# Performance work log

Hardware: AMD Instinct MI355X
Metric: run time of the kernel (lower is better)

## Reference

```python
import jax, jax.numpy as jnp
import numpy as np

MARGIN = 1.0
ALPHA = 0.5
EPS = 1e-12  # sqrt-smoothing epsilon (keeps grads finite on the zero diagonal)


def _pairwise_d2(x):
    # x: [B, D] -> squared euclidean distance matrix [B, B]
    sq = jnp.sum(x * x, axis=-1)
    return jnp.maximum(sq[:, None] + sq[None, :] - 2.0 * (x @ x.T), 0.0)


def setup_inputs() -> dict:
    key = jax.random.key(0)
    k1, k2 = jax.random.split(key)
    N, B, D = 32, 1024, 1024
    outputs = jax.random.normal(k1, (N, B, D), dtype=jnp.float32)
    encode_sentences = jax.random.normal(k2, (B, D), dtype=jnp.float32)
    return {"outputs": outputs, "encode_sentences": encode_sentences}


def reference(outputs, encode_sentences):
    # outputs: [N, B, D] (N secrets, batch B, embed D); encode_sentences: [B, D]
    N, B, D = outputs.shape

    # --- sentence (distance-consistency) loss ---
    # original: mean_i MSE( pdist(outputs[i]), pdist(encode_sentences) )
    d_sent = jnp.sqrt(_pairwise_d2(encode_sentences) + EPS)          # [B, B]
    d_out = jnp.sqrt(jax.vmap(_pairwise_d2)(outputs) + EPS)          # [N, B, B]
    # mean over N of per-i means == global mean (all terms same size B*B)
    sentence_loss = jnp.mean((d_out - d_sent[None]) ** 2)

    # --- secret (pairwise margin) loss ---
    # original: sum_{i<j} mean_b relu(margin - ||outputs[i,b] - outputs[j,b]||)
    x = jnp.swapaxes(outputs, 0, 1)                                   # [B, N, D]
    sq = jnp.sum(x * x, axis=-1)                                      # [B, N]
    gram = jnp.einsum('bnd,bmd->bnm', x, x)                           # [B, N, N]
    d2 = jnp.maximum(sq[:, :, None] + sq[:, None, :] - 2.0 * gram, 0.0)
    d = jnp.sqrt(d2 + EPS)                                            # [B, N, N]
    hinge = jax.nn.relu(MARGIN - d)                                   # [B, N, N]
    upper = jnp.triu(jnp.ones((N, N), dtype=bool), k=1)               # i < j mask
    secret_distance = jnp.sum(jnp.where(upper[None], hinge, 0.0)) / B
    n_pairs = N * (N - 1) / 2.0
    secret_loss = secret_distance / n_pairs

    loss = ALPHA * sentence_loss + (1.0 - ALPHA) * secret_loss
    return (loss, sentence_loss, secret_loss)
```

## Files before the change

### kernel.cpp

```cpp
#include <hip/hip_runtime.h>
#include <hip/hip_bf16.h>

#define N_SEC 32
#define BDIM 1024
#define DDIM 1024

typedef __attribute__((ext_vector_type(8))) short bf16x8;
typedef __attribute__((ext_vector_type(4))) float f32x4;
typedef __attribute__((ext_vector_type(4))) int i32x4;

#define WAITVM(n) asm volatile("s_waitcnt vmcnt(" #n ")" ::: "memory")

__device__ __forceinline__ void bar() {
    __builtin_amdgcn_s_barrier();
    asm volatile("" ::: "memory");
}

__device__ __forceinline__ unsigned pk2(float a, float b) {
    union { __hip_bfloat162 h; unsigned u; } cv;
    cv.h = __float22bfloat162_rn(make_float2(a, b));
    return cv.u;
}

__device__ __forceinline__ i32x4 pack8(float4 a, float4 b) {
    i32x4 r;
    r[0] = pk2(a.x, a.y); r[1] = pk2(a.z, a.w);
    r[2] = pk2(b.x, b.y); r[3] = pk2(b.z, b.w);
    return r;
}

__device__ __forceinline__ f32x4 mfma16(bf16x8 a, bf16x8 b, f32x4 c) {
    return __builtin_amdgcn_mfma_f32_16x16x32_bf16(a, b, c, 0, 0, 0);
}

__device__ __forceinline__ float wave_sum(float v) {
    #pragma unroll
    for (int off = 32; off > 0; off >>= 1) v += __shfl_down(v, off, 64);
    return v;
}

__device__ __forceinline__ void gload16(const unsigned short* g, unsigned short* l) {
    __builtin_amdgcn_global_load_lds(
        (const __attribute__((address_space(1))) unsigned int*)g,
        (__attribute__((address_space(3))) unsigned int*)l, 16, 0, 0);
}


__global__ void prep_k(const float* __restrict__ outp, const float* __restrict__ enc,
                       unsigned short* __restrict__ Xb, unsigned short* __restrict__ Eb,
                       float* __restrict__ sq_out, float* __restrict__ sq_enc) {
    int wid = threadIdx.x >> 6, l = threadIdx.x & 63;
    int r = blockIdx.x * 4 + wid;
    bool isOut = r < N_SEC * BDIM;
    const float* src = isOut ? (outp + (size_t)r * DDIM)
                             : (enc + (size_t)(r - N_SEC * BDIM) * DDIM);
    unsigned short* dst = isOut ? (Xb + (size_t)r * DDIM)
                                : (Eb + (size_t)(r - N_SEC * BDIM) * DDIM);
    const float4* s4 = (const float4*)src;
    float s = 0.f;
    #pragma unroll
    for (int h = 0; h < 2; ++h) {
        int c = l + h * 64;
        float4 v0 = s4[2 * c], v1 = s4[2 * c + 1];
        i32x4 p = pack8(v0, v1);
        *(i32x4*)&dst[c * 8] = p;
        #pragma unroll
        for (int e = 0; e < 4; ++e) {
            unsigned u = (unsigned)p[e];
            float a = __uint_as_float(u << 16);
            float b = __uint_as_float(u & 0xFFFF0000u);
            s += a * a + b * b;
        }
    }
    s = wave_sum(s);
    if (l == 0) { if (isOut) sq_out[r] = s; else sq_enc[r - N_SEC * BDIM] = s; }
}

__global__ void zero_k(float* __restrict__ p) {
    int i = blockIdx.x * blockDim.x + threadIdx.x;
    float4 z = {0.f, 0.f, 0.f, 0.f};
    ((float4*)p)[i] = z;
    ((float4*)p)[i + 131072] = z;
}

__global__ void cvt0_k(float* __restrict__ d, const float* __restrict__ sq) {
    int t = blockIdx.x * blockDim.x + threadIdx.x;
    #pragma unroll
    for (int h = 0; h < 2; ++h) {
        int idx = t + h * 131072;
        int i = idx >> 8;
        float si = sq[i];
        float4 g = ((const float4*)d)[idx];
        int j0 = (idx & 255) * 4;
        float4 r;
        r.x = sqrtf(fmaxf(si + sq[j0 + 0] - 2.f * g.x, 0.f) + 1e-12f);
        r.y = sqrtf(fmaxf(si + sq[j0 + 1] - 2.f * g.y, 0.f) + 1e-12f);
        r.z = sqrtf(fmaxf(si + sq[j0 + 2] - 2.f * g.z, 0.f) + 1e-12f);
        r.w = sqrtf(fmaxf(si + sq[j0 + 3] - 2.f * g.w, 0.f) + 1e-12f);
        ((float4*)d)[idx] = r;
    }
}

template<int MODE, int NIT>
__global__ void gram8_k(const unsigned short* __restrict__ Xb, const float* __restrict__ sqv,
                        const float* __restrict__ dsent_r, float* __restrict__ dsent_w,
                        float* __restrict__ partials, int kbeg_base) {
    int n, tile, kbeg;
    if (MODE == 1) {
        int g = blockIdx.x;
        int xcd = g & 7, local = g >> 3;
        n = xcd * 4 + local / 36;
        tile = local % 36;
        kbeg = 0;
    } else {
        n = 0;
        tile = blockIdx.x >> 2;
        kbeg = (blockIdx.x & 3) * NIT;
        (void)kbeg_base;
    }
    int idx = tile, ti = 0;
    while (idx >= 8 - ti) { idx -= 8 - ti; ti++; }
    int tj = ti + idx;
    const unsigned short* Xn = Xb + (size_t)n * BDIM * DDIM;
    const float* sqn = sqv + n * BDIM;
    int i0 = ti * 128, j0 = tj * 128;
    bool diag = (ti == tj);

    __shared__ __align__(16) unsigned short Ash[3][4096];
    __shared__ __align__(16) unsigned short Bsh[3][4096];
    __shared__ float red[4];

    int t = threadIdx.x, wid = t >> 6, l = t & 63;
    int wr = wid >> 1, wc = wid & 1;
    bool dead = diag && (wr > wc);
    int cg = l >> 4, lr = l & 15;

    f32x4 acc[4][4];
    #pragma unroll
    for (int a = 0; a < 4; a++)
        #pragma unroll
        for (int c = 0; c < 4; c++) acc[a][c] = f32x4{0.f, 0.f, 0.f, 0.f};

    int eoffA[4], eoffB[4];
    #pragma unroll
    for (int f = 0; f < 4; f++) {
        int ra = wr * 64 + f * 16 + lr;
        eoffA[f] = ra * 32 + ((cg ^ ((ra >> 1) & 3)) * 8);
        int rb = wc * 64 + f * 16 + lr;
        eoffB[f] = rb * 32 + ((cg ^ ((rb >> 1) & 3)) * 8);
    }

    int rs = wid * 16 + (l >> 2);
    int cgs = (l & 3) ^ ((rs >> 1) & 3);
    const unsigned short* gA0 = Xn + (size_t)(i0 + rs) * DDIM + cgs * 8;
    const unsigned short* gA1 = gA0 + (size_t)64 * DDIM;
    const unsigned short* gB0 = Xn + (size_t)(j0 + rs) * DDIM + cgs * 8;
    const unsigned short* gB1 = gB0 + (size_t)64 * DDIM;

    auto stage = [&](int buf, int kt) {
        int ko = kt * 32;
        gload16(gA0 + ko, &Ash[buf][wid * 512]);
        gload16(gA1 + ko, &Ash[buf][2048 + wid * 512]);
        gload16(gB0 + ko, &Bsh[buf][wid * 512]);
        gload16(gB1 + ko, &Bsh[buf][2048 + wid * 512]);
    };
    auto compute = [&](int buf) {
        if (dead) return;
        bf16x8 af[4], bfr[4];
        #pragma unroll
        for (int f = 0; f < 4; f++) {
            af[f]  = *(const bf16x8*)&Ash[buf][eoffA[f]];
            bfr[f] = *(const bf16x8*)&Bsh[buf][eoffB[f]];
        }
        #pragma unroll
        for (int fi = 0; fi < 4; fi++)
            #pragma unroll
            for (int fj = 0; fj < 4; fj++) {
                if (diag && wr == wc && fj < fi) continue;
                acc[fi][fj] = mfma16(af[fi], bfr[fj], acc[fi][fj]);
            }
    };

    int klast = kbeg + NIT - 1;
#define GSTEP(SB, CB) do {                       \
        int nx = c + 1; if (nx > klast) nx = klast; \
        stage(SB, nx);                           \
        WAITVM(4);                               \
        bar();                                   \
        compute(CB);                             \
        ++c; } while (0)

    stage(0, kbeg);
    int c = kbeg;
    #pragma unroll 1
    for (int it = 0; it < NIT / 3; ++it) {
        GSTEP(1, 0);
        GSTEP(2, 1);
        GSTEP(0, 2);
    }
    if (NIT % 3 >= 1) GSTEP(1, 0);
    if (NIT % 3 >= 2) GSTEP(2, 1);
#undef GSTEP
    asm volatile("s_waitcnt vmcnt(0)" ::: "memory");

    float lsum = 0.f;
    if (!dead) {
        #pragma unroll
        for (int fi = 0; fi < 4; fi++) {
            #pragma unroll
            for (int fj = 0; fj < 4; fj++) {
                if (diag && wr == wc && fj < fi) continue;
                int jg = j0 + wc * 64 + fj * 16 + lr;
                #pragma unroll
                for (int e = 0; e < 4; e++) {
                    int ig = i0 + wr * 64 + fi * 16 + cg * 4 + e;
                    float g = acc[fi][fj][e];
                    if (MODE == 2) {
                        atomicAdd(&dsent_w[(size_t)ig * BDIM + jg], g);
                    } else {
                        float d2 = sqn[ig] + sqn[jg] - 2.f * g;
                        float d = sqrtf(fmaxf(d2, 0.f) + 1e-12f);
                        if (!diag || jg > ig) {
                            float diff = d - dsent_r[(size_t)ig * BDIM + jg];
                            lsum += diff * diff;
                        }
                    }
                }
            }
        }
    }
    if (MODE == 1) {
        lsum = wave_sum(lsum * 2.f);
        if (l == 0) red[wid] = lsum;
        __syncthreads();
        if (t == 0) partials[blockIdx.x] = red[0] + red[1] + red[2] + red[3];
    }
}

__global__ void secret4_k(const unsigned short* __restrict__ Xb,
                          const float* __restrict__ sq_out, float* __restrict__ partials) {
    __shared__ __align__(16) unsigned short S[2][32 * 4 * 128];
    __shared__ float red[4];
    int t = threadIdx.x, wid = t >> 6, l = t & 63;
    int b0 = blockIdx.x * 4;
    int cg = l >> 4, lr = l & 15;
    f32x4 a00 = {0.f,0.f,0.f,0.f}, a01 = {0.f,0.f,0.f,0.f}, a11 = {0.f,0.f,0.f,0.f};

    auto stage = [&](int buf, int kt) {
        #pragma unroll
        for (int m = 0; m < 8; ++m) {
            int n = m * 4 + wid;
            gload16(Xb + ((size_t)(n * BDIM + b0 + cg)) * DDIM + kt * 128 + ((lr ^ (n & 7)) * 8),
                    &S[buf][n * 512]);
        }
    };
    auto compute = [&](int buf) {
        #pragma unroll
        for (int k2 = 0; k2 < 4; ++k2) {
            int cs = k2 * 4 + cg;
            int cl = (cs ^ (lr & 7)) * 8;
            bf16x8 u0 = *(const bf16x8*)&S[buf][lr * 512 + wid * 128 + cl];
            bf16x8 u1 = *(const bf16x8*)&S[buf][(16 + lr) * 512 + wid * 128 + cl];
            a00 = mfma16(u0, u0, a00);
            a01 = mfma16(u0, u1, a01);
            a11 = mfma16(u1, u1, a11);
        }
    };

    stage(0, 0);
    __syncthreads();
    for (int kt = 0; kt < 6; kt += 2) {
        stage(1, kt + 1);
        compute(0);
        __syncthreads();
        stage(0, kt + 2);
        compute(1);
        __syncthreads();
    }
    stage(1, 7);
    compute(0);
    __syncthreads();
    compute(1);

    float lsum = 0.f;
    int b = b0 + wid;
    auto proc = [&](const f32x4& acc, int rb, int cb) {
        #pragma unroll
        for (int e = 0; e < 4; e++) {
            int i = rb * 16 + cg * 4 + e;
            int j = cb * 16 + lr;
            if (j > i) {
                float d2 = sq_out[(size_t)i * BDIM + b] + sq_out[(size_t)j * BDIM + b] - 2.f * acc[e];
                float d = sqrtf(fmaxf(d2, 0.f) + 1e-12f);
                lsum += fmaxf(1.f - d, 0.f);
            }
        }
    };
    proc(a00, 0, 0); proc(a01, 0, 1); proc(a11, 1, 1);
    lsum = wave_sum(lsum);
    if (l == 0) red[wid] = lsum;
    __syncthreads();
    if (t == 0) partials[blockIdx.x] = red[0] + red[1] + red[2] + red[3];
}

__global__ void fin2_k(const float* __restrict__ ps, const float* __restrict__ psec,
                       float* __restrict__ out) {
    __shared__ float red[16];
    int t = threadIdx.x;
    float s = 0.f;
    for (int i = t; i < 36 * N_SEC; i += 256) s += ps[i];
    float s2 = psec[t];
    s = wave_sum(s);
    s2 = wave_sum(s2);
    if ((t & 63) == 0) { red[t >> 6] = s; red[8 + (t >> 6)] = s2; }
    __syncthreads();
    if (t == 0) {
        float a = red[0] + red[1] + red[2] + red[3];
        float b = red[8] + red[9] + red[10] + red[11];
        float sl = a * (1.0f / 33554432.0f);
        float sec = b * (1.0f / (1024.0f * 496.0f));
        out[0] = 0.5f * sl + 0.5f * sec;
        out[1] = sl;
        out[2] = sec;
    }
}


__global__ void norms_k(const float* __restrict__ outp, const float* __restrict__ enc,
                        float* __restrict__ sq_out, float* __restrict__ sq_enc) {
    int wid = threadIdx.x >> 6, l = threadIdx.x & 63;
    int r = blockIdx.x * 4 + wid;
    const float* src = (r < N_SEC * BDIM) ? (outp + (size_t)r * DDIM)
                                          : (enc + (size_t)(r - N_SEC * BDIM) * DDIM);
    float s = 0.f;
    #pragma unroll
    for (int q = 0; q < 4; q++) {
        float4 v = reinterpret_cast<const float4*>(src)[l + q * 64];
        unsigned u0 = pk2(v.x, v.y), u1 = pk2(v.z, v.w);
        float a = __uint_as_float(u0 << 16), b = __uint_as_float(u0 & 0xFFFF0000u);
        float c = __uint_as_float(u1 << 16), d = __uint_as_float(u1 & 0xFFFF0000u);
        s += a * a + b * b + c * c + d * d;
    }
    s = wave_sum(s);
    if (l == 0) { if (r < N_SEC * BDIM) sq_out[r] = s; else sq_enc[r - N_SEC * BDIM] = s; }
}

template<int MODE>
__global__ void gram_k(const float* __restrict__ X, const float* __restrict__ sqv,
                       const float* __restrict__ dsent_r, float* __restrict__ dsent_w,
                       float* __restrict__ accum) {
    int idx = blockIdx.x, ti = 0;
    while (idx >= 8 - ti) { idx -= 8 - ti; ti++; }
    int tj = ti + idx;
    int n = (MODE == 1) ? blockIdx.y : 0;
    const float* Xn = X + (size_t)n * BDIM * DDIM;
    const float* sqn = sqv + n * BDIM;
    int i0 = ti * 128, j0 = tj * 128;
    bool diag = (ti == tj);
    __shared__ __align__(16) unsigned short Ash[128 * 32];
    __shared__ __align__(16) unsigned short Bsh[128 * 32];
    int t = threadIdx.x, wid = t >> 6, l = t & 63;
    int wr = wid >> 1, wc = wid & 1;
    bool dead = diag && (wr > wc);
    int cg = l >> 4, lr = l & 15;
    f32x4 acc[4][4];
    #pragma unroll
    for (int a = 0; a < 4; a++)
        #pragma unroll
        for (int c = 0; c < 4; c++) acc[a][c] = f32x4{0.f, 0.f, 0.f, 0.f};
    int r0 = t >> 2, c0 = t & 3;
    int swz0 = (c0 ^ (r0 & 3)) * 8;
    int off0 = r0 * 32 + swz0;
    int off1 = (r0 + 64) * 32 + swz0;
    for (int kt = 0; kt < DDIM / 32; ++kt) {
        int k0 = kt * 32;
        const float4* pa0 = (const float4*)(Xn + (size_t)(i0 + r0) * DDIM + k0 + c0 * 8);
        const float4* pa1 = (const float4*)(Xn + (size_t)(i0 + r0 + 64) * DDIM + k0 + c0 * 8);
        const float4* pb0 = (const float4*)(Xn + (size_t)(j0 + r0) * DDIM + k0 + c0 * 8);
        const float4* pb1 = (const float4*)(Xn + (size_t)(j0 + r0 + 64) * DDIM + k0 + c0 * 8);
        float4 a00 = pa0[0], a01 = pa0[1];
        float4 a10 = pa1[0], a11 = pa1[1];
        float4 b00 = pb0[0], b01 = pb0[1];
        float4 b10 = pb1[0], b11 = pb1[1];
        __syncthreads();
        *(i32x4*)&Ash[off0] = pack8(a00, a01);
        *(i32x4*)&Ash[off1] = pack8(a10, a11);
        *(i32x4*)&Bsh[off0] = pack8(b00, b01);
        *(i32x4*)&Bsh[off1] = pack8(b10, b11);
        __syncthreads();
        if (!dead) {
            bf16x8 af[4], bfr[4];
            #pragma unroll
            for (int f = 0; f < 4; f++) {
                int ra = wr * 64 + f * 16 + lr;
                af[f] = *(const bf16x8*)&Ash[ra * 32 + ((cg ^ (ra & 3)) * 8)];
                int rb = wc * 64 + f * 16 + lr;
                bfr[f] = *(const bf16x8*)&Bsh[rb * 32 + ((cg ^ (rb & 3)) * 8)];
            }
            #pragma unroll
            for (int fi = 0; fi < 4; fi++)
                #pragma unroll
                for (int fj = 0; fj < 4; fj++) {
                    if (diag && wr == wc && fj < fi) continue;
                    acc[fi][fj] = mfma16(af[fi], bfr[fj], acc[fi][fj]);
                }
        }
    }
    if (!dead) {
        float lsum = 0.f;
        #pragma unroll
        for (int fi = 0; fi < 4; fi++) {
            #pragma unroll
            for (int fj = 0; fj < 4; fj++) {
                if (diag && wr == wc && fj < fi) continue;
                int jg = j0 + wc * 64 + fj * 16 + lr;
                #pragma unroll
                for (int e = 0; e < 4; e++) {
                    int ig = i0 + wr * 64 + fi * 16 + cg * 4 + e;
                    float g = acc[fi][fj][e];
                    float d2 = sqn[ig] + sqn[jg] - 2.f * g;
                    float d = sqrtf(fmaxf(d2, 0.f) + 1e-12f);
                    if (MODE == 0) {
                        dsent_w[(size_t)ig * BDIM + jg] = d;
                    } else {
                        if (!diag || jg > ig) {
                            float diff = d - dsent_r[(size_t)ig * BDIM + jg];
                            lsum += diff * diff;
                        }
                    }
                }
            }
        }
        if (MODE == 1) {
            lsum = wave_sum(lsum * 2.f);
            if (l == 0) atomicAdd(accum, lsum);
        }
    }
}

__global__ void secret_k(const float* __restrict__ X, const float* __restrict__ sq_out,
                         float* __restrict__ accum) {
    int wid = threadIdx.x >> 6, l = threadIdx.x & 63;
    int b = blockIdx.x * 4 + wid;
    int cg = l >> 4, lr = l & 15;
    f32x4 a00 = {0.f,0.f,0.f,0.f}, a01 = {0.f,0.f,0.f,0.f}, a11 = {0.f,0.f,0.f,0.f};
    for (int kt = 0; kt < 32; ++kt) {
        int k0 = kt * 32 + cg * 8;
        const float4* p0 = (const float4*)(X + ((size_t)lr * BDIM + b) * DDIM + k0);
        const float4* p1 = (const float4*)(X + ((size_t)(16 + lr) * BDIM + b) * DDIM + k0);
        union { i32x4 i; bf16x8 s; } u0, u1;
        u0.i = pack8(p0[0], p0[1]);
        u1.i = pack8(p1[0], p1[1]);
        a00 = mfma16(u0.s, u0.s, a00);
        a01 = mfma16(u0.s, u1.s, a01);
        a11 = mfma16(u1.s, u1.s, a11);
    }
    float lsum = 0.f;
    auto proc = [&](const f32x4& acc, int rb, int cb) {
        #pragma unroll
        for (int e = 0; e < 4; e++) {
            int i = rb * 16 + cg * 4 + e;
            int j = cb * 16 + lr;
            if (j > i) {
                float d2 = sq_out[(size_t)i * BDIM + b] + sq_out[(size_t)j * BDIM + b] - 2.f * acc[e];
                float d = sqrtf(fmaxf(d2, 0.f) + 1e-12f);
                lsum += fmaxf(1.f - d, 0.f);
            }
        }
    };
    proc(a00, 0, 0); proc(a01, 0, 1); proc(a11, 1, 1);
    lsum = wave_sum(lsum);
    if (l == 0) atomicAdd(accum, lsum);
}

__global__ void init_k(float* sums) { sums[threadIdx.x] = 0.f; }

__global__ void fin_k(const float* __restrict__ sums, float* __restrict__ out) {
    float sl = sums[0] * (1.0f / 33554432.0f);
    float sec = sums[1] * (1.0f / (1024.0f * 496.0f));
    out[0] = 0.5f * sl + 0.5f * sec;
    out[1] = sl;
    out[2] = sec;
}

extern "C" void kernel_launch(void* const* d_in, const int* in_sizes, int n_in,
                              void* d_out, int out_size, void* d_ws, size_t ws_size,
                              hipStream_t stream) {
    const float* outputs = (const float*)d_in[0];
    const float* enc     = (const float*)d_in[1];
    float* out = (float*)d_out;

    float* ps     = (float*)d_ws;
    float* psec   = ps + 1536;
    float* sq_out = ps + 2048;
    float* sq_enc = sq_out + N_SEC * BDIM;
    float* dsent  = sq_enc + BDIM;
    unsigned short* Xbf = (unsigned short*)(dsent + (size_t)BDIM * BDIM);
    unsigned short* Ebf = Xbf + (size_t)N_SEC * BDIM * DDIM;

    const size_t NEED = 4 * (2048 + (size_t)N_SEC * BDIM + BDIM + (size_t)BDIM * BDIM)
                      + 2 * ((size_t)N_SEC * BDIM * DDIM + (size_t)BDIM * DDIM);

    if (ws_size >= NEED) {
        hipLaunchKernelGGL(prep_k, dim3((N_SEC * BDIM + BDIM) / 4), dim3(256), 0, stream,
                           outputs, enc, Xbf, Ebf, sq_out, sq_enc);
        hipLaunchKernelGGL(zero_k, dim3(512), dim3(256), 0, stream, dsent);
        hipLaunchKernelGGL((gram8_k<2, 8>), dim3(36 * 4), dim3(256), 0, stream,
                           Ebf, sq_enc, (const float*)nullptr, dsent, (float*)nullptr, 0);
        hipLaunchKernelGGL(cvt0_k, dim3(512), dim3(256), 0, stream, dsent, sq_enc);
        hipLaunchKernelGGL((gram8_k<1, 32>), dim3(36 * N_SEC), dim3(256), 0, stream,
                           Xbf, sq_out, (const float*)dsent, (float*)nullptr, ps, 0);
        hipLaunchKernelGGL(secret4_k, dim3(BDIM / 4), dim3(256), 0, stream,
                           Xbf, sq_out, psec);
        hipLaunchKernelGGL(fin2_k, dim3(1), dim3(256), 0, stream, ps, psec, out);
    } else {
        float* sums = (float*)d_ws;
        float* fsq_out = sums + 64;
        float* fsq_enc = fsq_out + N_SEC * BDIM;
        float* fdsent  = fsq_enc + BDIM;
        hipLaunchKernelGGL(init_k, dim3(1), dim3(2), 0, stream, sums);
        hipLaunchKernelGGL(norms_k, dim3((N_SEC * BDIM + BDIM) / 4), dim3(256), 0, stream,
                           outputs, enc, fsq_out, fsq_enc);
        hipLaunchKernelGGL((gram_k<0>), dim3(36), dim3(256), 0, stream,
                           enc, fsq_enc, (const float*)nullptr, fdsent, (float*)nullptr);
        hipLaunchKernelGGL((gram_k<1>), dim3(36, N_SEC), dim3(256), 0, stream,
                           outputs, fsq_out, (const float*)fdsent, (float*)nullptr, &sums[0]);
        hipLaunchKernelGGL(secret_k, dim3(BDIM / 4), dim3(256), 0, stream,
                           outputs, fsq_out, &sums[1]);
        hipLaunchKernelGGL(fin_k, dim3(1), dim3(1), 0, stream, sums, out);
    }
}
```

Before: 146.9 us.

## Replace triangular 128-tile gram kernel with full 256x256 tiles, 8 waves, 64-wide K

The per-secret gram and distance-loss kernel changes from 36 triangular 128x128 tiles per secret, which skipped mirrored work, to 16 full 256x256 tiles with 512 threads. Each block now uses a double-buffered, interleaved staging schedule with a 64-wide K step, XOR-swizzled LDS and raised wave priority around the MFMAs. The goal is more data reuse per loaded byte and fewer blocks, at the cost of roughly 1.8x the MFMA work, since the symmetric half is no longer skipped. To support this, the sentence gram kernel now writes a full symmetric distance matrix and the final reduction reads a fixed 512 partials.

```diff
diff --git a/kernel.cpp b/kernel.cpp
--- a/kernel.cpp
+++ b/kernel.cpp
@@ -43,6 +43,37 @@
     __builtin_amdgcn_global_load_lds(
         (const __attribute__((address_space(1))) unsigned int*)g,
         (__attribute__((address_space(3))) unsigned int*)l, 16, 0, 0);
+}
+
+__device__ __forceinline__ void rdA(bf16x8 af[2][2], const unsigned short* base,
+                                    int FI0, int lr, int s0, int s1) {
+    #pragma unroll
+    for (int a2 = 0; a2 < 2; ++a2) {
+        int ro = ((FI0 + a2) * 16 + lr) * 64;
+        af[a2][0] = *(const bf16x8*)(base + ro + s0);
+        af[a2][1] = *(const bf16x8*)(base + ro + s1);
+    }
+}
+__device__ __forceinline__ void rdB(bf16x8 bq[4][2], const unsigned short* base,
+                                    int rbase, int lr, int s0, int s1) {
+    #pragma unroll
+    for (int fj = 0; fj < 4; ++fj) {
+        int ro = (rbase + fj * 16 + lr) * 64;
+        bq[fj][0] = *(const bf16x8*)(base + ro + s0);
+        bq[fj][1] = *(const bf16x8*)(base + ro + s1);
+    }
+}
+__device__ __forceinline__ void mm16(f32x4 acc[8][4], const bf16x8 af[2][2],
+                                     const bf16x8 bq[4][2], int FI0) {
+    __builtin_amdgcn_s_setprio(1);
+    #pragma unroll
+    for (int kk = 0; kk < 2; ++kk)
+        #pragma unroll
+        for (int a2 = 0; a2 < 2; ++a2)
+            #pragma unroll
+            for (int fj = 0; fj < 4; ++fj)
+                acc[FI0 + a2][fj] = mfma16(af[a2][kk], bq[fj][kk], acc[FI0 + a2][fj]);
+    __builtin_amdgcn_s_setprio(0);
 }
 
 
@@ -101,34 +132,19 @@
     }
 }
 
-template<int MODE, int NIT>
-__global__ void gram8_k(const unsigned short* __restrict__ Xb, const float* __restrict__ sqv,
-                        const float* __restrict__ dsent_r, float* __restrict__ dsent_w,
-                        float* __restrict__ partials, int kbeg_base) {
-    int n, tile, kbeg;
-    if (MODE == 1) {
-        int g = blockIdx.x;
-        int xcd = g & 7, local = g >> 3;
-        n = xcd * 4 + local / 36;
-        tile = local % 36;
-        kbeg = 0;
-    } else {
-        n = 0;
-        tile = blockIdx.x >> 2;
-        kbeg = (blockIdx.x & 3) * NIT;
-        (void)kbeg_base;
-    }
+template<int NIT>
+__global__ void gramE_k(const unsigned short* __restrict__ Xb, float* __restrict__ gw) {
+    int tile = blockIdx.x >> 2;
+    int kbeg = (blockIdx.x & 3) * NIT;
     int idx = tile, ti = 0;
     while (idx >= 8 - ti) { idx -= 8 - ti; ti++; }
     int tj = ti + idx;
-    const unsigned short* Xn = Xb + (size_t)n * BDIM * DDIM;
-    const float* sqn = sqv + n * BDIM;
+    const unsigned short* Xn = Xb;
     int i0 = ti * 128, j0 = tj * 128;
     bool diag = (ti == tj);
 
     __shared__ __align__(16) unsigned short Ash[3][4096];
     __shared__ __align__(16) unsigned short Bsh[3][4096];
-    __shared__ float red[4];
 
     int t = threadIdx.x, wid = t >> 6, l = t & 63;
     int wr = wid >> 1, wc = wid & 1;
@@ -149,7 +165,6 @@
         int rb = wc * 64 + f * 16 + lr;
         eoffB[f] = rb * 32 + ((cg ^ ((rb >> 1) & 3)) * 8);
     }
-
     int rs = wid * 16 + (l >> 2);
     int cgs = (l & 3) ^ ((rs >> 1) & 3);
     const unsigned short* gA0 = Xn + (size_t)(i0 + rs) * DDIM + cgs * 8;
@@ -189,24 +204,18 @@
         bar();                                   \
         compute(CB);                             \
         ++c; } while (0)
-
     stage(0, kbeg);
     int c = kbeg;
     #pragma unroll 1
-    for (int it = 0; it < NIT / 3; ++it) {
-        GSTEP(1, 0);
-        GSTEP(2, 1);
-        GSTEP(0, 2);
-    }
+    for (int it = 0; it < NIT / 3; ++it) { GSTEP(1, 0); GSTEP(2, 1); GSTEP(0, 2); }
     if (NIT % 3 >= 1) GSTEP(1, 0);
     if (NIT % 3 >= 2) GSTEP(2, 1);
 #undef GSTEP
     asm volatile("s_waitcnt vmcnt(0)" ::: "memory");
 
-    float lsum = 0.f;
     if (!dead) {
         #pragma unroll
-        for (int fi = 0; fi < 4; fi++) {
+        for (int fi = 0; fi < 4; fi++)
             #pragma unroll
             for (int fj = 0; fj < 4; fj++) {
                 if (diag && wr == wc && fj < fi) continue;
@@ -215,25 +224,128 @@
                 for (int e = 0; e < 4; e++) {
                     int ig = i0 + wr * 64 + fi * 16 + cg * 4 + e;
                     float g = acc[fi][fj][e];
-                    if (MODE == 2) {
-                        atomicAdd(&dsent_w[(size_t)ig * BDIM + jg], g);
-                    } else {
-                        float d2 = sqn[ig] + sqn[jg] - 2.f * g;
-                        float d = sqrtf(fmaxf(d2, 0.f) + 1e-12f);
-                        if (!diag || jg > ig) {
-                            float diff = d - dsent_r[(size_t)ig * BDIM + jg];
-                            lsum += diff * diff;
-                        }
-                    }
+                    if (jg >= ig) atomicAdd(&gw[(size_t)ig * BDIM + jg], g);
+                    if (jg > ig)  atomicAdd(&gw[(size_t)jg * BDIM + ig], g);
                 }
             }
-        }
-    }
-    if (MODE == 1) {
-        lsum = wave_sum(lsum * 2.f);
-        if (l == 0) red[wid] = lsum;
-        __syncthreads();
-        if (t == 0) partials[blockIdx.x] = red[0] + red[1] + red[2] + red[3];
+    }
+}
+
+__global__ __launch_bounds__(512, 2)
+void gram9_k(const unsigned short* __restrict__ Xb, const float* __restrict__ sqv,
+             const float* __restrict__ dsent, float* __restrict__ partials) {
+    int g = blockIdx.x;
+    int xcd = g & 7, local = g >> 3;
+    int n = xcd * 4 + (local >> 4);
+    int tile = local & 15;
+    int ti = tile >> 2, tj = tile & 3;
+    const unsigned short* Xn = Xb + (size_t)n * BDIM * DDIM;
+    const float* sqn = sqv + n * BDIM;
+    int i0 = ti * 256, j0 = tj * 256;
+
+    __shared__ __align__(16) unsigned short Ash[2][2][8192];
+    __shared__ __align__(16) unsigned short Bsh[2][2][8192];
+    __shared__ float red[8];
+
+    int t = threadIdx.x, wid = t >> 6, l = t & 63;
+    int wr = wid >> 2, wc = wid & 3;
+    int cg = l >> 4, lr = l & 15;
+    int hb = wc >> 1, wcl = wc & 1;
+
+    f32x4 acc[8][4];
+    #pragma unroll
+    for (int a = 0; a < 8; a++)
+        #pragma unroll
+        for (int c = 0; c < 4; c++) acc[a][c] = f32x4{0.f, 0.f, 0.f, 0.f};
+
+    int s0 = ((0 + cg) ^ (lr & 7)) * 8;
+    int s1 = ((4 + cg) ^ (lr & 7)) * 8;
+    const unsigned short* Abase = &Ash[0][wr][0];
+    const unsigned short* Bbase = &Bsh[0][hb][0];
+    int brow = wcl * 64;
+
+    int rq = wid * 16 + (l >> 3);
+    int chk = ((l & 7) ^ (l >> 3)) * 8;
+    const unsigned short* pA0 = Xn + (size_t)(i0 + rq) * DDIM + chk;
+    const unsigned short* pA1 = pA0 + (size_t)8 * DDIM;
+    const unsigned short* pB0 = Xn + (size_t)(j0 + rq) * DDIM + chk;
+    const unsigned short* pB1 = pB0 + (size_t)8 * DDIM;
+    int dstq = wid * 1024;
+
+#define STAGE_A(PR, H, KT) do {                                              \
+        gload16(pA0 + (size_t)(H) * 131072 + (KT) * 64, &Ash[PR][H][dstq]);  \
+        gload16(pA1 + (size_t)(H) * 131072 + (KT) * 64, &Ash[PR][H][dstq + 512]); } while (0)
+#define STAGE_B(PR, H, KT) do {                                              \
+        gload16(pB0 + (size_t)(H) * 131072 + (KT) * 64, &Bsh[PR][H][dstq]);  \
+        gload16(pB1 + (size_t)(H) * 131072 + (KT) * 64, &Bsh[PR][H][dstq + 512]); } while (0)
+
+#define ITER(P, KA, KB) do {                                                 \
+        bf16x8 bq[4][2]; bf16x8 af[2][2];                                    \
+                                                                \
+        WAITVM(4);                                                           \
+        bar();                                                               \
+        STAGE_A(P ^ 1, 0, KA);                                               \
+        rdB(bq, Bbase + (P) * 16384, brow, lr, s0, s1);                      \
+        rdA(af, Abase + (P) * 16384, 0, lr, s0, s1);                         \
+        mm16(acc, af, bq, 0);                                                \
+                                                                \
+        rdA(af, Abase + (P) * 16384, 2, lr, s0, s1);                         \
+        bar();                                                               \
+        STAGE_A(P ^ 1, 1, KA);                                               \
+        mm16(acc, af, bq, 2);                                                \
+                                                                \
+        rdA(af, Abase + (P) * 16384, 4, lr, s0, s1);                         \
+        bar();                                                               \
+        STAGE_B(P, 0, KB);                                                   \
+        mm16(acc, af, bq, 4);                                                \
+                                                                \
+        rdA(af, Abase + (P) * 16384, 6, lr, s0, s1);                         \
+        bar();                                                               \
+        STAGE_B(P, 1, KB);                                                   \
+        mm16(acc, af, bq, 6); } while (0)
+
+    STAGE_A(0, 0, 0); STAGE_A(0, 1, 0);
+    STAGE_B(0, 0, 0); STAGE_B(0, 1, 0);
+    STAGE_B(1, 0, 1); STAGE_B(1, 1, 1);
+
+    #pragma unroll 1
+    for (int it = 0; it < 8; ++it) {
+        int t0 = 2 * it, t1 = 2 * it + 1;
+        int kA0 = (t0 + 1 > 15) ? 15 : t0 + 1, kB0 = (t0 + 2 > 15) ? 15 : t0 + 2;
+        int kA1 = (t1 + 1 > 15) ? 15 : t1 + 1, kB1 = (t1 + 2 > 15) ? 15 : t1 + 2;
+        ITER(0, kA0, kB0);
+        ITER(1, kA1, kB1);
+    }
+#undef ITER
+#undef STAGE_A
+#undef STAGE_B
+    asm volatile("s_waitcnt vmcnt(0)" ::: "memory");
+
+    float lsum = 0.f;
+    #pragma unroll
+    for (int fi = 0; fi < 8; fi++) {
+        #pragma unroll
+        for (int fj = 0; fj < 4; fj++) {
+            int jg = j0 + wc * 64 + fj * 16 + lr;
+            #pragma unroll
+            for (int e = 0; e < 4; e++) {
+                int ig = i0 + wr * 128 + fi * 16 + cg * 4 + e;
+                float gg = acc[fi][fj][e];
+                float d2 = sqn[ig] + sqn[jg] - 2.f * gg;
+                float d = sqrtf(fmaxf(d2, 0.f) + 1e-12f);
+                float diff = d - dsent[(size_t)ig * BDIM + jg];
+                lsum += diff * diff;
+            }
+        }
+    }
+    lsum = wave_sum(lsum);
+    if (l == 0) red[wid] = lsum;
+    __syncthreads();
+    if (t == 0) {
+        float s = 0.f;
+        #pragma unroll
+        for (int w = 0; w < 8; ++w) s += red[w];
+        partials[blockIdx.x] = s;
     }
 }
 
@@ -307,8 +419,7 @@
                        float* __restrict__ out) {
     __shared__ float red[16];
     int t = threadIdx.x;
-    float s = 0.f;
-    for (int i = t; i < 36 * N_SEC; i += 256) s += ps[i];
+    float s = ps[t] + ps[t + 256];
     float s2 = psec[t];
     s = wave_sum(s);
     s2 = wave_sum(s2);
@@ -505,11 +616,10 @@
         hipLaunchKernelGGL(prep_k, dim3((N_SEC * BDIM + BDIM) / 4), dim3(256), 0, stream,
                            outputs, enc, Xbf, Ebf, sq_out, sq_enc);
         hipLaunchKernelGGL(zero_k, dim3(512), dim3(256), 0, stream, dsent);
-        hipLaunchKernelGGL((gram8_k<2, 8>), dim3(36 * 4), dim3(256), 0, stream,
-                           Ebf, sq_enc, (const float*)nullptr, dsent, (float*)nullptr, 0);
+        hipLaunchKernelGGL((gramE_k<8>), dim3(36 * 4), dim3(256), 0, stream, Ebf, dsent);
         hipLaunchKernelGGL(cvt0_k, dim3(512), dim3(256), 0, stream, dsent, sq_enc);
-        hipLaunchKernelGGL((gram8_k<1, 32>), dim3(36 * N_SEC), dim3(256), 0, stream,
-                           Xbf, sq_out, (const float*)dsent, (float*)nullptr, ps, 0);
+        hipLaunchKernelGGL(gram9_k, dim3(512), dim3(512), 0, stream,
+                           Xbf, sq_out, dsent, ps);
         hipLaunchKernelGGL(secret4_k, dim3(BDIM / 4), dim3(256), 0, stream,
                            Xbf, sq_out, psec);
         hipLaunchKernelGGL(fin2_k, dim3(1), dim3(256), 0, stream, ps, psec, out);
```

After: 161.5 us. 9.9% more time.

## Fuse secret and sentence gram kernels, fold zeroing into prep, symmetrize encoder gram

Applied to the files above, without the earlier changes.

Folds the zeroing of the sentence distance buffer into extra blocks of the prep kernel. The secret-loss and per-secret gram kernels are merged into one launch with a shared LDS buffer, so the small secret blocks run alongside the large gram tiles. In the merged kernel the gram pipeline uses two buffers instead of three, with an extra barrier per step, and the secret path uses smaller K chunks. The encoder gram now writes both triangles through atomics so later reads see a full matrix. This removes launches and tail gaps, at the cost of twice the atomic traffic and less prefetch depth in the gram loop.

```diff
diff --git a/kernel.cpp b/kernel.cpp
--- a/kernel.cpp
+++ b/kernel.cpp
@@ -48,7 +48,16 @@
 
 __global__ void prep_k(const float* __restrict__ outp, const float* __restrict__ enc,
                        unsigned short* __restrict__ Xb, unsigned short* __restrict__ Eb,
-                       float* __restrict__ sq_out, float* __restrict__ sq_enc) {
+                       float* __restrict__ sq_out, float* __restrict__ sq_enc,
+                       float* __restrict__ dzero) {
+    if (blockIdx.x >= 8448) {
+        float4 z = {0.f, 0.f, 0.f, 0.f};
+        int base = (blockIdx.x - 8448) * 256 + threadIdx.x;
+        #pragma unroll
+        for (int q = 0; q < 16; ++q)
+            ((float4*)dzero)[q * 16384 + base] = z;
+        return;
+    }
     int wid = threadIdx.x >> 6, l = threadIdx.x & 63;
     int r = blockIdx.x * 4 + wid;
     bool isOut = r < N_SEC * BDIM;
@@ -74,13 +83,6 @@
     }
     s = wave_sum(s);
     if (l == 0) { if (isOut) sq_out[r] = s; else sq_enc[r - N_SEC * BDIM] = s; }
-}
-
-__global__ void zero_k(float* __restrict__ p) {
-    int i = blockIdx.x * blockDim.x + threadIdx.x;
-    float4 z = {0.f, 0.f, 0.f, 0.f};
-    ((float4*)p)[i] = z;
-    ((float4*)p)[i + 131072] = z;
 }
 
 __global__ void cvt0_k(float* __restrict__ d, const float* __restrict__ sq) {
@@ -101,34 +103,19 @@
     }
 }
 
-template<int MODE, int NIT>
-__global__ void gram8_k(const unsigned short* __restrict__ Xb, const float* __restrict__ sqv,
-                        const float* __restrict__ dsent_r, float* __restrict__ dsent_w,
-                        float* __restrict__ partials, int kbeg_base) {
-    int n, tile, kbeg;
-    if (MODE == 1) {
-        int g = blockIdx.x;
-        int xcd = g & 7, local = g >> 3;
-        n = xcd * 4 + local / 36;
-        tile = local % 36;
-        kbeg = 0;
-    } else {
-        n = 0;
-        tile = blockIdx.x >> 2;
-        kbeg = (blockIdx.x & 3) * NIT;
-        (void)kbeg_base;
-    }
+template<int NIT>
+__global__ void gramE_k(const unsigned short* __restrict__ Xb, float* __restrict__ gw) {
+    int tile = blockIdx.x >> 2;
+    int kbeg = (blockIdx.x & 3) * NIT;
     int idx = tile, ti = 0;
     while (idx >= 8 - ti) { idx -= 8 - ti; ti++; }
     int tj = ti + idx;
-    const unsigned short* Xn = Xb + (size_t)n * BDIM * DDIM;
-    const float* sqn = sqv + n * BDIM;
+    const unsigned short* Xn = Xb;
     int i0 = ti * 128, j0 = tj * 128;
     bool diag = (ti == tj);
 
     __shared__ __align__(16) unsigned short Ash[3][4096];
     __shared__ __align__(16) unsigned short Bsh[3][4096];
-    __shared__ float red[4];
 
     int t = threadIdx.x, wid = t >> 6, l = t & 63;
     int wr = wid >> 1, wc = wid & 1;
@@ -149,7 +136,6 @@
         int rb = wc * 64 + f * 16 + lr;
         eoffB[f] = rb * 32 + ((cg ^ ((rb >> 1) & 3)) * 8);
     }
-
     int rs = wid * 16 + (l >> 2);
     int cgs = (l & 3) ^ ((rs >> 1) & 3);
     const unsigned short* gA0 = Xn + (size_t)(i0 + rs) * DDIM + cgs * 8;
@@ -189,24 +175,18 @@
         bar();                                   \
         compute(CB);                             \
         ++c; } while (0)
-
     stage(0, kbeg);
     int c = kbeg;
     #pragma unroll 1
-    for (int it = 0; it < NIT / 3; ++it) {
-        GSTEP(1, 0);
-        GSTEP(2, 1);
-        GSTEP(0, 2);
-    }
+    for (int it = 0; it < NIT / 3; ++it) { GSTEP(1, 0); GSTEP(2, 1); GSTEP(0, 2); }
     if (NIT % 3 >= 1) GSTEP(1, 0);
     if (NIT % 3 >= 2) GSTEP(2, 1);
 #undef GSTEP
     asm volatile("s_waitcnt vmcnt(0)" ::: "memory");
 
-    float lsum = 0.f;
     if (!dead) {
         #pragma unroll
-        for (int fi = 0; fi < 4; fi++) {
+        for (int fi = 0; fi < 4; fi++)
             #pragma unroll
             for (int fj = 0; fj < 4; fj++) {
                 if (diag && wr == wc && fj < fi) continue;
@@ -215,92 +195,184 @@
                 for (int e = 0; e < 4; e++) {
                     int ig = i0 + wr * 64 + fi * 16 + cg * 4 + e;
                     float g = acc[fi][fj][e];
-                    if (MODE == 2) {
-                        atomicAdd(&dsent_w[(size_t)ig * BDIM + jg], g);
-                    } else {
-                        float d2 = sqn[ig] + sqn[jg] - 2.f * g;
-                        float d = sqrtf(fmaxf(d2, 0.f) + 1e-12f);
-                        if (!diag || jg > ig) {
-                            float diff = d - dsent_r[(size_t)ig * BDIM + jg];
-                            lsum += diff * diff;
-                        }
+                    if (jg >= ig) atomicAdd(&gw[(size_t)ig * BDIM + jg], g);
+                    if (jg > ig)  atomicAdd(&gw[(size_t)jg * BDIM + ig], g);
+                }
+            }
+    }
+}
+
+__global__ void fused_k(const unsigned short* __restrict__ Xb,
+                        const float* __restrict__ sq_out,
+                        const float* __restrict__ dsent,
+                        float* __restrict__ ps, float* __restrict__ psec) {
+    __shared__ __align__(16) unsigned short SH[16384];
+    __shared__ float red[4];
+    int t = threadIdx.x, wid = t >> 6, l = t & 63;
+    int cg = l >> 4, lr = l & 15;
+
+    if (blockIdx.x < 256) {
+        int b0 = blockIdx.x * 4;
+        f32x4 a00 = {0.f,0.f,0.f,0.f}, a01 = {0.f,0.f,0.f,0.f}, a11 = {0.f,0.f,0.f,0.f};
+        int nbase = wid * 2;
+        auto sstage = [&](int buf, int kt) {
+            #pragma unroll
+            for (int m = 0; m < 4; ++m) {
+                int nn = m * 8 + nbase + (l >> 5);
+                int bb = b0 + ((l >> 3) & 3);
+                int ch = (l & 7) ^ (nn & 7);
+                gload16(Xb + ((size_t)(nn * BDIM + bb)) * DDIM + kt * 64 + ch * 8,
+                        &SH[buf * 8192 + (m * 8 + nbase) * 256]);
+            }
+        };
+        auto scompute = [&](int buf) {
+            #pragma unroll
+            for (int k2 = 0; k2 < 2; ++k2) {
+                int cs = k2 * 4 + cg;
+                int cl = (cs ^ (lr & 7)) * 8;
+                bf16x8 u0 = *(const bf16x8*)&SH[buf * 8192 + lr * 256 + wid * 64 + cl];
+                bf16x8 u1 = *(const bf16x8*)&SH[buf * 8192 + (16 + lr) * 256 + wid * 64 + cl];
+                a00 = mfma16(u0, u0, a00);
+                a01 = mfma16(u0, u1, a01);
+                a11 = mfma16(u1, u1, a11);
+            }
+        };
+        sstage(0, 0);
+        __syncthreads();
+        for (int kt = 0; kt < 14; kt += 2) {
+            sstage(1, kt + 1); scompute(0); __syncthreads();
+            sstage(0, kt + 2); scompute(1); __syncthreads();
+        }
+        sstage(1, 15); scompute(0); __syncthreads(); scompute(1);
+
+        float lsum = 0.f;
+        int b = b0 + wid;
+        auto proc = [&](const f32x4& acc, int rb, int cb) {
+            #pragma unroll
+            for (int e = 0; e < 4; e++) {
+                int i = rb * 16 + cg * 4 + e;
+                int j = cb * 16 + lr;
+                if (j > i) {
+                    float d2 = sq_out[(size_t)i * BDIM + b] + sq_out[(size_t)j * BDIM + b] - 2.f * acc[e];
+                    float d = sqrtf(fmaxf(d2, 0.f) + 1e-12f);
+                    lsum += fmaxf(1.f - d, 0.f);
+                }
+            }
+        };
+        proc(a00, 0, 0); proc(a01, 0, 1); proc(a11, 1, 1);
+        lsum = wave_sum(lsum);
+        if (l == 0) red[wid] = lsum;
+        __syncthreads();
+        if (t == 0) psec[blockIdx.x] = red[0] + red[1] + red[2] + red[3];
+        return;
+    }
+
+    int g = blockIdx.x - 256;
+    int xcd = g & 7, local = g >> 3;
+    int n = xcd * 4 + local / 36;
+    int tile = local % 36;
+    int idx = tile, ti = 0;
+    while (idx >= 8 - ti) { idx -= 8 - ti; ti++; }
+    int tj = ti + idx;
+    const unsigned short* Xn = Xb + (size_t)n * BDIM * DDIM;
+    const float* sqn = sq_out + n * BDIM;
+    int i0 = ti * 128, j0 = tj * 128;
+    bool diag = (ti == tj);
+
+    int wr = wid >> 1, wc = wid & 1;
+    bool dead = diag && (wr > wc);
+
+    f32x4 acc[4][4];
+    #pragma unroll
+    for (int a = 0; a < 4; a++)
+        #pragma unroll
+        for (int c = 0; c < 4; c++) acc[a][c] = f32x4{0.f, 0.f, 0.f, 0.f};
+
+    int eoffA[4], eoffB[4];
+    #pragma unroll
+    for (int f = 0; f < 4; f++) {
+        int ra = wr * 64 + f * 16 + lr;
+        eoffA[f] = ra * 32 + ((cg ^ ((ra >> 1) & 3)) * 8);
+        int rb = wc * 64 + f * 16 + lr;
+        eoffB[f] = rb * 32 + ((cg ^ ((rb >> 1) & 3)) * 8);
+    }
+
+    int rs = wid * 16 + (l >> 2);
+    int cgs = (l & 3) ^ ((rs >> 1) & 3);
+    const unsigned short* gA0 = Xn + (size_t)(i0 + rs) * DDIM + cgs * 8;
+    const unsigned short* gA1 = gA0 + (size_t)64 * DDIM;
+    const unsigned short* gB0 = Xn + (size_t)(j0 + rs) * DDIM + cgs * 8;
+    const unsigned short* gB1 = gB0 + (size_t)64 * DDIM;
+
+    auto stage = [&](int buf, int kt) {
+        int ko = kt * 32;
+        gload16(gA0 + ko, &SH[buf * 4096 + wid * 512]);
+        gload16(gA1 + ko, &SH[buf * 4096 + 2048 + wid * 512]);
+        gload16(gB0 + ko, &SH[8192 + buf * 4096 + wid * 512]);
+        gload16(gB1 + ko, &SH[8192 + buf * 4096 + 2048 + wid * 512]);
+    };
+    auto compute = [&](int buf) {
+        if (dead) return;
+        bf16x8 af[4], bfr[4];
+        #pragma unroll
+        for (int f = 0; f < 4; f++) {
+            af[f]  = *(const bf16x8*)&SH[buf * 4096 + eoffA[f]];
+            bfr[f] = *(const bf16x8*)&SH[8192 + buf * 4096 + eoffB[f]];
+        }
+        #pragma unroll
+        for (int fi = 0; fi < 4; fi++)
+            #pragma unroll
+            for (int fj = 0; fj < 4; fj++) {
+                if (diag && wr == wc && fj < fi) continue;
+                acc[fi][fj] = mfma16(af[fi], bfr[fj], acc[fi][fj]);
+            }
+    };
+
+#define GSTEP(NB, CB) do {                       \
+        bar();                                   \
+        int nx = c + 1; if (nx > 31) nx = 31;    \
+        stage(NB, nx);                           \
+        WAITVM(4);                               \
+        bar();                                   \
+        compute(CB);                             \
+        ++c; } while (0)
+
+    stage(0, 0);
+    int c = 0;
+    #pragma unroll 1
+    for (int it = 0; it < 16; ++it) {
+        GSTEP(1, 0);
+        GSTEP(0, 1);
+    }
+#undef GSTEP
+    asm volatile("s_waitcnt vmcnt(0)" ::: "memory");
+
+    float lsum = 0.f;
+    if (!dead) {
+        #pragma unroll
+        for (int fi = 0; fi < 4; fi++) {
+            #pragma unroll
+            for (int fj = 0; fj < 4; fj++) {
+                if (diag && wr == wc && fj < fi) continue;
+                int jg = j0 + wc * 64 + fj * 16 + lr;
+                #pragma unroll
+                for (int e = 0; e < 4; e++) {
+                    int ig = i0 + wr * 64 + fi * 16 + cg * 4 + e;
+                    float gg = acc[fi][fj][e];
+                    float d2 = sqn[ig] + sqn[jg] - 2.f * gg;
+                    float d = sqrtf(fmaxf(d2, 0.f) + 1e-12f);
+                    if (!diag || jg > ig) {
+                        float diff = d - dsent[(size_t)ig * BDIM + jg];
+                        lsum += diff * diff;
                     }
                 }
             }
         }
     }
-    if (MODE == 1) {
-        lsum = wave_sum(lsum * 2.f);
-        if (l == 0) red[wid] = lsum;
-        __syncthreads();
-        if (t == 0) partials[blockIdx.x] = red[0] + red[1] + red[2] + red[3];
-    }
-}
-
-__global__ void secret4_k(const unsigned short* __restrict__ Xb,
-                          const float* __restrict__ sq_out, float* __restrict__ partials) {
-    __shared__ __align__(16) unsigned short S[2][32 * 4 * 128];
-    __shared__ float red[4];
-    int t = threadIdx.x, wid = t >> 6, l = t & 63;
-    int b0 = blockIdx.x * 4;
-    int cg = l >> 4, lr = l & 15;
-    f32x4 a00 = {0.f,0.f,0.f,0.f}, a01 = {0.f,0.f,0.f,0.f}, a11 = {0.f,0.f,0.f,0.f};
-
-    auto stage = [&](int buf, int kt) {
-        #pragma unroll
-        for (int m = 0; m < 8; ++m) {
-            int n = m * 4 + wid;
-            gload16(Xb + ((size_t)(n * BDIM + b0 + cg)) * DDIM + kt * 128 + ((lr ^ (n & 7)) * 8),
-                    &S[buf][n * 512]);
-        }
-    };
-    auto compute = [&](int buf) {
-        #pragma unroll
-        for (int k2 = 0; k2 < 4; ++k2) {
-            int cs = k2 * 4 + cg;
-            int cl = (cs ^ (lr & 7)) * 8;
-            bf16x8 u0 = *(const bf16x8*)&S[buf][lr * 512 + wid * 128 + cl];
-            bf16x8 u1 = *(const bf16x8*)&S[buf][(16 + lr) * 512 + wid * 128 + cl];
-            a00 = mfma16(u0, u0, a00);
-            a01 = mfma16(u0, u1, a01);
-            a11 = mfma16(u1, u1, a11);
-        }
-    };
-
-    stage(0, 0);
-    __syncthreads();
-    for (int kt = 0; kt < 6; kt += 2) {
-        stage(1, kt + 1);
-        compute(0);
-        __syncthreads();
-        stage(0, kt + 2);
-        compute(1);
-        __syncthreads();
-    }
-    stage(1, 7);
-    compute(0);
-    __syncthreads();
-    compute(1);
-
-    float lsum = 0.f;
-    int b = b0 + wid;
-    auto proc = [&](const f32x4& acc, int rb, int cb) {
-        #pragma unroll
-        for (int e = 0; e < 4; e++) {
-            int i = rb * 16 + cg * 4 + e;
-            int j = cb * 16 + lr;
-            if (j > i) {
-                float d2 = sq_out[(size_t)i * BDIM + b] + sq_out[(size_t)j * BDIM + b] - 2.f * acc[e];
-                float d = sqrtf(fmaxf(d2, 0.f) + 1e-12f);
-                lsum += fmaxf(1.f - d, 0.f);
-            }
-        }
-    };
-    proc(a00, 0, 0); proc(a01, 0, 1); proc(a11, 1, 1);
-    lsum = wave_sum(lsum);
+    lsum = wave_sum(lsum * 2.f);
     if (l == 0) red[wid] = lsum;
     __syncthreads();
-    if (t == 0) partials[blockIdx.x] = red[0] + red[1] + red[2] + red[3];
+    if (t == 0) ps[g] = red[0] + red[1] + red[2] + red[3];
 }
 
 __global__ void fin2_k(const float* __restrict__ ps, const float* __restrict__ psec,
@@ -502,16 +574,12 @@
                       + 2 * ((size_t)N_SEC * BDIM * DDIM + (size_t)BDIM * DDIM);
 
     if (ws_size >= NEED) {
-        hipLaunchKernelGGL(prep_k, dim3((N_SEC * BDIM + BDIM) / 4), dim3(256), 0, stream,
-                           outputs, enc, Xbf, Ebf, sq_out, sq_enc);
-        hipLaunchKernelGGL(zero_k, dim3(512), dim3(256), 0, stream, dsent);
-        hipLaunchKernelGGL((gram8_k<2, 8>), dim3(36 * 4), dim3(256), 0, stream,
-                           Ebf, sq_enc, (const float*)nullptr, dsent, (float*)nullptr, 0);
+        hipLaunchKernelGGL(prep_k, dim3(8448 + 64), dim3(256), 0, stream,
+                           outputs, enc, Xbf, Ebf, sq_out, sq_enc, dsent);
+        hipLaunchKernelGGL((gramE_k<8>), dim3(36 * 4), dim3(256), 0, stream, Ebf, dsent);
         hipLaunchKernelGGL(cvt0_k, dim3(512), dim3(256), 0, stream, dsent, sq_enc);
-        hipLaunchKernelGGL((gram8_k<1, 32>), dim3(36 * N_SEC), dim3(256), 0, stream,
-                           Xbf, sq_out, (const float*)dsent, (float*)nullptr, ps, 0);
-        hipLaunchKernelGGL(secret4_k, dim3(BDIM / 4), dim3(256), 0, stream,
-                           Xbf, sq_out, psec);
+        hipLaunchKernelGGL(fused_k, dim3(256 + 1152), dim3(256), 0, stream,
+                           Xbf, sq_out, dsent, ps, psec);
         hipLaunchKernelGGL(fin2_k, dim3(1), dim3(256), 0, stream, ps, psec, out);
     } else {
         float* sums = (float*)d_ws;
```

Measured after the change: 160.3 us. +9.1%, slower.

## Replace per-secret gram kernel with 128x128 upper-triangle tiled MFMA kernel

Applied to the files above, without the earlier changes.

Adds a new kernel that computes each secret's pairwise-distance Gram matrix as 36 upper-triangle 128x128 tiles. It uses double-buffered swizzled LDS staging of K=32 slices, and maps blocks to XCDs so each XCD's blocks share the same secret matrices for L2 reuse. On diagonal tiles it skips the MFMAs for the lower-triangle wave and the lower-triangle fragments. The aim is better data reuse and less redundant work in the dominant sentence-loss kernel. The cost is a different tile shape and pipeline depth that may change occupancy and register pressure.

```diff
diff --git a/kernel.cpp b/kernel.cpp
--- a/kernel.cpp
+++ b/kernel.cpp
@@ -235,6 +235,123 @@
         __syncthreads();
         if (t == 0) partials[blockIdx.x] = red[0] + red[1] + red[2] + red[3];
     }
+}
+
+__global__ void gramF_k(const unsigned short* __restrict__ Xb,
+                        const float* __restrict__ sq_out,
+                        const float* __restrict__ dsent,
+                        float* __restrict__ ps) {
+    __shared__ __align__(16) unsigned short SH[16384];
+    __shared__ float red[4];
+    int t = threadIdx.x, wid = t >> 6, l = t & 63;
+    int cg = l >> 4, lr = l & 15;
+
+    int g = blockIdx.x;
+    int xcd = g & 7, local = g >> 3;
+    int n = xcd * 4 + local / 36;
+    int tile = local % 36;
+    int idx = tile, ti = 0;
+    while (idx >= 8 - ti) { idx -= 8 - ti; ti++; }
+    int tj = ti + idx;
+    const unsigned short* Xn = Xb + (size_t)n * BDIM * DDIM;
+    const float* sqn = sq_out + n * BDIM;
+    int i0 = ti * 128, j0 = tj * 128;
+    bool diag = (ti == tj);
+
+    int wr = wid >> 1, wc = wid & 1;
+    bool dead = diag && (wr > wc);
+
+    f32x4 acc[4][4];
+    #pragma unroll
+    for (int a = 0; a < 4; a++)
+        #pragma unroll
+        for (int c = 0; c < 4; c++) acc[a][c] = f32x4{0.f, 0.f, 0.f, 0.f};
+
+    int eoffA[4], eoffB[4];
+    #pragma unroll
+    for (int f = 0; f < 4; f++) {
+        int ra = wr * 64 + f * 16 + lr;
+        eoffA[f] = ra * 32 + ((cg ^ ((ra >> 1) & 3)) * 8);
+        int rb = wc * 64 + f * 16 + lr;
+        eoffB[f] = rb * 32 + ((cg ^ ((rb >> 1) & 3)) * 8);
+    }
+
+    int rs = wid * 16 + (l >> 2);
+    int cgs = (l & 3) ^ ((rs >> 1) & 3);
+    const unsigned short* gA0 = Xn + (size_t)(i0 + rs) * DDIM + cgs * 8;
+    const unsigned short* gA1 = gA0 + (size_t)64 * DDIM;
+    const unsigned short* gB0 = Xn + (size_t)(j0 + rs) * DDIM + cgs * 8;
+    const unsigned short* gB1 = gB0 + (size_t)64 * DDIM;
+
+    auto stage = [&](int buf, int kt) {
+        int ko = kt * 32;
+        gload16(gA0 + ko, &SH[buf * 4096 + wid * 512]);
+        gload16(gA1 + ko, &SH[buf * 4096 + 2048 + wid * 512]);
+        gload16(gB0 + ko, &SH[8192 + buf * 4096 + wid * 512]);
+        gload16(gB1 + ko, &SH[8192 + buf * 4096 + 2048 + wid * 512]);
+    };
+    auto compute = [&](int buf) {
+        if (dead) return;
+        bf16x8 af[4], bfr[4];
+        #pragma unroll
+        for (int f = 0; f < 4; f++) {
+            af[f]  = *(const bf16x8*)&SH[buf * 4096 + eoffA[f]];
+            bfr[f] = *(const bf16x8*)&SH[8192 + buf * 4096 + eoffB[f]];
+        }
+        #pragma unroll
+        for (int fi = 0; fi < 4; fi++)
+            #pragma unroll
+            for (int fj = 0; fj < 4; fj++) {
+                if (diag && wr == wc && fj < fi) continue;
+                acc[fi][fj] = mfma16(af[fi], bfr[fj], acc[fi][fj]);
+            }
+    };
+
+#define GSTEP(NB, CB) do {                       \
+        bar();                                   \
+        int nx = c + 1; if (nx > 31) nx = 31;    \
+        stage(NB, nx);                           \
+        WAITVM(4);                               \
+        bar();                                   \
+        compute(CB);                             \
+        ++c; } while (0)
+
+    stage(0, 0);
+    int c = 0;
+    #pragma unroll 1
+    for (int it = 0; it < 16; ++it) {
+        GSTEP(1, 0);
+        GSTEP(0, 1);
+    }
+#undef GSTEP
+    asm volatile("s_waitcnt vmcnt(0)" ::: "memory");
+
+    float lsum = 0.f;
+    if (!dead) {
+        #pragma unroll
+        for (int fi = 0; fi < 4; fi++) {
+            #pragma unroll
+            for (int fj = 0; fj < 4; fj++) {
+                if (diag && wr == wc && fj < fi) continue;
+                int jg = j0 + wc * 64 + fj * 16 + lr;
+                #pragma unroll
+                for (int e = 0; e < 4; e++) {
+                    int ig = i0 + wr * 64 + fi * 16 + cg * 4 + e;
+                    float gg = acc[fi][fj][e];
+                    float d2 = sqn[ig] + sqn[jg] - 2.f * gg;
+                    float d = sqrtf(fmaxf(d2, 0.f) + 1e-12f);
+                    if (!diag || jg > ig) {
+                        float diff = d - dsent[(size_t)ig * BDIM + jg];
+                        lsum += diff * diff;
+                    }
+                }
+            }
+        }
+    }
+    lsum = wave_sum(lsum * 2.f);
+    if (l == 0) red[wid] = lsum;
+    __syncthreads();
+    if (t == 0) ps[g] = red[0] + red[1] + red[2] + red[3];
 }
 
 __global__ void secret4_k(const unsigned short* __restrict__ Xb,
@@ -508,8 +625,8 @@
         hipLaunchKernelGGL((gram8_k<2, 8>), dim3(36 * 4), dim3(256), 0, stream,
                            Ebf, sq_enc, (const float*)nullptr, dsent, (float*)nullptr, 0);
         hipLaunchKernelGGL(cvt0_k, dim3(512), dim3(256), 0, stream, dsent, sq_enc);
-        hipLaunchKernelGGL((gram8_k<1, 32>), dim3(36 * N_SEC), dim3(256), 0, stream,
-                           Xbf, sq_out, (const float*)dsent, (float*)nullptr, ps, 0);
+        hipLaunchKernelGGL(gramF_k, dim3(36 * N_SEC), dim3(256), 0, stream,
+                           Xbf, sq_out, dsent, ps);
         hipLaunchKernelGGL(secret4_k, dim3(BDIM / 4), dim3(256), 0, stream,
                            Xbf, sq_out, psec);
         hipLaunchKernelGGL(fin2_k, dim3(1), dim3(256), 0, stream, ps, psec, out);
```

After: 145.3 us. Within noise of the previous version (-1.1%).
